# Kernel optimization log

Hardware: AMD Instinct MI355X
Metric: run time of the kernel (lower is better)

The kernel has to match this reference:

```python
import jax, jax.numpy as jnp
import numpy as np
from jax import lax

B, C, H, W = 32, 64, 56, 56
G = 4            # num_heads*2 with num_heads=2
SMK, K = 5, 7
C2 = C // 2
HEAD_DIM = C // G
SCALE = HEAD_DIM ** -0.5


def _bias_idx(k, h, w):
    # static replica of ContMix.generate_idx + apply_rpb index construction
    rpb_size = 2 * k - 1
    idx_h = np.arange(k)
    idx_w = np.arange(k)
    idx_k = (idx_h[:, None] * rpb_size + idx_w).reshape(-1)
    rep_h = np.ones(k, np.int64); rep_h[k // 2] = h - (k - 1)
    rep_w = np.ones(k, np.int64); rep_w[k // 2] = w - (k - 1)
    bias_hw = np.repeat(idx_h, rep_h)[:, None] * rpb_size + np.repeat(idx_w, rep_w)  # (h, w)
    bias_idx = (bias_hw[..., None] + idx_k).reshape(-1, k * k)[::-1]  # torch.flip dim 0
    return jnp.asarray(bias_idx.copy())

IDX1 = _bias_idx(SMK, H, W)
IDX2 = _bias_idx(K, H, W)


def setup_inputs() -> dict:
    key = jax.random.key(0)
    ks = jax.random.split(key, 18)
    r = lambda i, sh: jax.random.normal(ks[i], sh, jnp.float32)
    return dict(
        x=r(0, (B, C, H, W)),
        lepe_w=r(1, (C, 1, K, K)) * 0.1,
        lepe_b=r(2, (C,)) * 0.1,
        lepe_bn_s=1.0 + 0.1 * r(3, (C,)),
        lepe_bn_b=0.1 * r(4, (C,)),
        wq_w=r(5, (C2, C2)) * (C2 ** -0.5),
        wq_bn_s=1.0 + 0.1 * r(6, (C2,)),
        wq_bn_b=0.1 * r(7, (C2,)),
        wk_w=r(8, (C2, C2)) * (C2 ** -0.5),
        wk_bn_s=1.0 + 0.1 * r(9, (C2,)),
        wk_bn_b=0.1 * r(10, (C2,)),
        wp_w=r(11, (SMK * SMK + K * K, 49)) * (49 ** -0.5),
        wp_b=0.1 * r(12, (SMK * SMK + K * K,)),
        rpb1=0.02 * r(13, (G, 2 * SMK - 1, 2 * SMK - 1)),
        rpb2=0.02 * r(14, (G, 2 * K - 1, 2 * K - 1)),
        dy_w=r(15, (C, C)) * (C ** -0.5),
        dy_bn_s=1.0 + 0.1 * r(16, (C,)),
        dy_bn_b=0.1 * r(17, (C,)),
    )


def _per_ch(t):
    return t[None, :, None, None]


def _contmix(x, lepe_w, lepe_b, lepe_bn_s, lepe_bn_b, wq_w, wq_bn_s, wq_bn_b,
             wk_w, wk_bn_s, wk_bn_b, wp_w, wp_b, rpb1, rpb2, dy_w, dy_bn_s, dy_bn_b):
    # lepe: deploy-mode DilatedReparamBlock = depthwise 7x7 conv (+bias), then eval BN
    lepe = lax.conv_general_dilated(x, lepe_w, (1, 1), [(K // 2, K // 2)] * 2,
                                    feature_group_count=C)
    lepe = (lepe + _per_ch(lepe_b)) * _per_ch(lepe_bn_s) + _per_ch(lepe_bn_b)

    q, kf = jnp.split(x, 2, axis=1)                         # (B, C2, H, W) each
    q = jnp.einsum('oi,bihw->bohw', wq_w, q)                # weight_query 1x1 conv
    q = (q * _per_ch(wq_bn_s) + _per_ch(wq_bn_b)) * SCALE
    # weight_key: AdaptiveAvgPool2d(7) -> 1x1 conv -> BN (H,W divisible by 7)
    kp = kf.reshape(B, C2, 7, H // 7, 7, W // 7).mean(axis=(3, 5))
    kp = jnp.einsum('oi,bihw->bohw', wk_w, kp)
    kp = kp * _per_ch(wk_bn_s) + _per_ch(wk_bn_b)

    qg = q.reshape(B, G, C2 // G, H * W)                    # b g c n
    kg = kp.reshape(B, G, C2 // G, 49)                      # b g c l
    w = jnp.einsum('bgcn,bgcl->bgnl', qg, kg)               # (B, G, HW, 49)
    # weight_proj: 1x1 conv over the 49 pooled-context channels
    w = jnp.einsum('ml,bgnl->bgnm', wp_w, w) + wp_b         # (B, G, HW, 74)
    w = w.reshape(B, G, H, W, SMK * SMK + K * K)

    attn1 = w[..., :SMK * SMK]
    attn2 = w[..., SMK * SMK:]
    attn1 = attn1 + rpb1.reshape(G, -1)[:, IDX1].reshape(1, G, H, W, SMK * SMK)
    attn2 = attn2 + rpb2.reshape(G, -1)[:, IDX2].reshape(1, G, H, W, K * K)
    attn1 = jax.nn.softmax(attn1, axis=-1)
    attn2 = jax.nn.softmax(attn2, axis=-1)

    c = C // (2 * G)                                        # value head dim = 8
    v = x.reshape(B, 2, G, c, H, W)                         # 'b (m g c) h w'

    def dyn_mix(attn, val, k):
        # unfold + einsum: content-adaptive depthwise mixing
        p = lax.conv_general_dilated_patches(
            val.reshape(B, G * c, H, W), (k, k), (1, 1), [(k // 2, k // 2)] * 2,
            dimension_numbers=('NCHW', 'OIHW', 'NCHW'))
        p = p.reshape(B, G, c, k * k, H, W)                 # channel-major patch layout
        return jnp.einsum('bgckhw,bghwk->bgchw', p, attn)

    x1 = dyn_mix(attn1, v[:, 0], SMK)
    x2 = dyn_mix(attn2, v[:, 1], K)
    out = jnp.concatenate([x1, x2], axis=1).reshape(B, C, H, W)
    out = jnp.einsum('oi,bihw->bohw', dy_w, out)            # dyconv_proj 1x1 + BN
    out = out * _per_ch(dy_bn_s) + _per_ch(dy_bn_b)
    return out + lepe


def reference(x, lepe_w, lepe_b, lepe_bn_s, lepe_bn_b, wq_w, wq_bn_s, wq_bn_b,
              wk_w, wk_bn_s, wk_bn_b, wp_w, wp_b, rpb1, rpb2, dy_w, dy_bn_s, dy_bn_b):
    return _contmix(x, lepe_w, lepe_b, lepe_bn_s, lepe_bn_b, wq_w, wq_bn_s, wq_bn_b,
                    wk_w, wk_bn_s, wk_bn_b, wp_w, wp_b, rpb1, rpb2, dy_w, dy_bn_s, dy_bn_b)
```

## Files before the change

### kernel.cpp

```cpp
#include <hip/hip_runtime.h>

#define BB 32
#define CC 64
#define HH 56
#define WW 56
#define HW 3136
#define TW 64
#define TR 12

__global__ __launch_bounds__(256) void prep_k(const float* __restrict__ x,
                                              const float* __restrict__ wk,
                                              const float* __restrict__ wks,
                                              const float* __restrict__ wkb,
                                              const float* __restrict__ wp_w,
                                              float* __restrict__ WK) {
    __shared__ float p_s[32 * 49];
    __shared__ float kg_s[8 * 49];
    const int b = blockIdx.x >> 2;
    const int g = blockIdx.x & 3;
    const int tid = threadIdx.x;
    for (int idx = tid; idx < 1568; idx += 256) {
        const int i = idx / 49, l = idx % 49;
        const int py = l / 7, px = l % 7;
        const float4* xp4 = reinterpret_cast<const float4*>(
            x + ((long)(b * CC + 32 + i)) * HW + py * 8 * WW + px * 8);
        float4 sA = make_float4(0.f, 0.f, 0.f, 0.f);
        float4 sB = make_float4(0.f, 0.f, 0.f, 0.f);
        #pragma unroll
        for (int y = 0; y < 8; ++y) {
            const float4 a = xp4[y * 14];
            const float4 c = xp4[y * 14 + 1];
            sA.x += a.x; sA.y += a.y; sA.z += a.z; sA.w += a.w;
            sB.x += c.x; sB.y += c.y; sB.z += c.z; sB.w += c.w;
        }
        p_s[idx] = (sA.x + sA.y + sA.z + sA.w + sB.x + sB.y + sB.z + sB.w) * (1.f / 64.f);
    }
    __syncthreads();
    for (int idx = tid; idx < 392; idx += 256) {
        const int o8 = idx / 49, l = idx % 49;
        const int o = g * 8 + o8;
        float acc = 0.f;
        #pragma unroll
        for (int i = 0; i < 32; ++i) acc = fmaf(wk[o * 32 + i], p_s[i * 49 + l], acc);
        kg_s[idx] = acc * wks[o] + wkb[o];
    }
    __syncthreads();
    for (int idx = tid; idx < 640; idx += 256) {
        const int c = idx / 80, slot = idx % 80;
        float acc = 0.f;
        int m = -1;
        if (slot < 28) { if (slot < 25) m = slot; }
        else           { if (slot < 77) m = 25 + (slot - 28); }
        if (m >= 0) {
            const float* kp = kg_s + c * 49;
            #pragma unroll
            for (int l = 0; l < 49; ++l) acc = fmaf(wp_w[m * 49 + l], kp[l], acc);
        }
        const long base = (long)blockIdx.x * 640;
        if (slot < 28) WK[base + c * 28 + slot] = acc;
        else           WK[base + 224 + c * 52 + (slot - 28)] = acc;
    }
}

__global__ __launch_bounds__(256) void attnmix_k(const float* __restrict__ x,
                                                 const float* __restrict__ WK,
                                                 const float* __restrict__ wq_w,
                                                 const float* __restrict__ wq_s,
                                                 const float* __restrict__ wq_bb,
                                                 const float* __restrict__ wp_b,
                                                 const float* __restrict__ rpb1,
                                                 const float* __restrict__ rpb2,
                                                 const float* __restrict__ lw,
                                                 const float* __restrict__ lb,
                                                 const float* __restrict__ ls,
                                                 const float* __restrict__ lbb,
                                                 float* __restrict__ mix,
                                                 float* __restrict__ out) {
    __shared__ float tile[8 * TR * TW];
    __shared__ float WK1_s[8 * 28];
    __shared__ float WK2_s[8 * 52];
    __shared__ float wqT_s[32 * 8];
    __shared__ float wpb1_s[25];
    __shared__ float wpb2_s[49];
    __shared__ float rpb1_s[81];
    __shared__ float rpb2_s[169];
    __shared__ float wqbn_s[16];
    __shared__ float lw_s[16 * 49];
    __shared__ float lbn_s[48];
    const int tid = threadIdx.x;
    const int bg = blockIdx.y;
    const int g = bg & 3, b = bg >> 2;

    {
        const float* wkp = WK + (long)bg * 640;
        for (int i = tid; i < 224; i += 256) WK1_s[i] = wkp[i];
        for (int i = tid; i < 416; i += 256) WK2_s[i] = wkp[224 + i];
    }
    {
        const int i = tid >> 3, c = tid & 7;
        wqT_s[tid] = wq_w[(g * 8 + c) * 32 + i];
    }
    if (tid < 25) wpb1_s[tid] = wp_b[tid];
    if (tid >= 32 && tid < 81) wpb2_s[tid - 32] = wp_b[25 + tid - 32];
    if (tid < 81) rpb1_s[tid] = rpb1[g * 81 + tid];
    if (tid < 169) rpb2_s[tid] = rpb2[g * 169 + tid];
    if (tid >= 192 && tid < 200) wqbn_s[tid - 192] = wq_s[g * 8 + tid - 192];
    if (tid >= 200 && tid < 208) wqbn_s[8 + tid - 200] = wq_bb[g * 8 + tid - 200];
    for (int i = tid; i < 784; i += 256) {
        const int ch = i / 49, k = i % 49;
        const int c = (ch < 8) ? (g * 8 + ch) : (32 + g * 8 + ch - 8);
        lw_s[i] = lw[c * 49 + k];
    }
    if (tid < 16) {
        const int c = (tid < 8) ? (g * 8 + tid) : (32 + g * 8 + tid - 8);
        lbn_s[tid] = lb[c]; lbn_s[16 + tid] = ls[c]; lbn_s[32 + tid] = lbb[c];
    }

    const int N0 = blockIdx.x << 8;
    const int ph0 = N0 / WW;
    const int r0 = ph0 - 3;

    {
        const float* xc = x + ((long)b * CC + g * 8) * HW;
        #pragma unroll
        for (int ch = 0; ch < 8; ++ch)
            for (int k = tid; k < TR * TW; k += 256) {
                const int row = k >> 6, lxx = k & 63;
                const int gy = r0 + row, gx = lxx - 3;
                float v = 0.f;
                if ((unsigned)gy < HH && (unsigned)gx < WW) v = xc[ch * HW + gy * WW + gx];
                tile[ch * (TR * TW) + k] = v;
            }
    }
    __syncthreads();

    const int n = N0 + tid;
    const bool valid = n < HW;
    const int nc = valid ? n : HW - 1;
    const int ph = nc / WW, pw = nc % WW;
    const int yr = HH - 1 - ph, xr = WW - 1 - pw;
    const int lrow = ph - r0;
    const int tb0 = (lrow - 3) * TW + pw;

    const float* xb = x + (long)b * CC * HW + nc;

    float q8[8];
    #pragma unroll
    for (int c = 0; c < 8; ++c) q8[c] = 0.f;
    for (int i = 0; i < 32; ++i) {
        const float xv = xb[i * HW];
        #pragma unroll
        for (int c = 0; c < 8; ++c) q8[c] = fmaf(wqT_s[i * 8 + c], xv, q8[c]);
    }
    #pragma unroll
    for (int c = 0; c < 8; ++c)
        q8[c] = (q8[c] * wqbn_s[c] + wqbn_s[8 + c]) * 0.25f;

    __builtin_amdgcn_sched_barrier(0);

    {
        float w1[25];
        #pragma unroll
        for (int m = 0; m < 25; ++m) w1[m] = wpb1_s[m];
        #pragma unroll
        for (int c = 0; c < 8; ++c) {
            const float qv = q8[c];
            #pragma unroll
            for (int m = 0; m < 25; ++m) w1[m] = fmaf(qv, WK1_s[c * 28 + m], w1[m]);
        }
        const int rh5 = yr < 2 ? yr : (yr > 53 ? yr - 51 : 2);
        const int rw5 = xr < 2 ? xr : (xr > 53 ? xr - 51 : 2);
        #pragma unroll
        for (int i = 0; i < 5; ++i)
            #pragma unroll
            for (int j = 0; j < 5; ++j)
                w1[i * 5 + j] += rpb1_s[(rh5 + i) * 9 + (rw5 + j)];
        float mx = -1e30f;
        #pragma unroll
        for (int m = 0; m < 25; ++m) mx = fmaxf(mx, w1[m]);
        float sm = 0.f;
        #pragma unroll
        for (int m = 0; m < 25; ++m) { w1[m] = __expf(w1[m] - mx); sm += w1[m]; }
        const float r = 1.f / sm;
        #pragma unroll
        for (int m = 0; m < 25; ++m) w1[m] *= r;

        float* m0 = mix + ((long)b * CC + g * 8) * HW + nc;
        float* o0 = out + ((long)b * CC + g * 8) * HW + nc;
        #pragma unroll
        for (int ch = 0; ch < 8; ++ch) {
            const float* t = tile + ch * (TR * TW) + tb0;
            const float* lwc = lw_s + ch * 49;
            float a = 0.f, la = 0.f;
            #pragma unroll
            for (int i = 0; i < 7; ++i)
                #pragma unroll
                for (int j = 0; j < 7; ++j) {
                    const float v = t[i * TW + j];
                    la = fmaf(lwc[i * 7 + j], v, la);
                    if (i >= 1 && i <= 5 && j >= 1 && j <= 5)
                        a = fmaf(w1[(i - 1) * 5 + (j - 1)], v, a);
                }
            if (valid) {
                m0[ch * HW] = a;
                o0[ch * HW] = (la + lbn_s[ch]) * lbn_s[16 + ch] + lbn_s[32 + ch];
            }
        }
    }

    __syncthreads();
    {
        const float* xc = x + ((long)b * CC + 32 + g * 8) * HW;
        #pragma unroll
        for (int ch = 0; ch < 8; ++ch)
            for (int k = tid; k < TR * TW; k += 256) {
                const int row = k >> 6, lxx = k & 63;
                const int gy = r0 + row, gx = lxx - 3;
                float v = 0.f;
                if ((unsigned)gy < HH && (unsigned)gx < WW) v = xc[ch * HW + gy * WW + gx];
                tile[ch * (TR * TW) + k] = v;
            }
    }
    __syncthreads();

    {
        float w2[49];
        #pragma unroll
        for (int m = 0; m < 49; ++m) w2[m] = wpb2_s[m];
        #pragma unroll
        for (int c = 0; c < 8; ++c) {
            const float qv = q8[c];
            #pragma unroll
            for (int m = 0; m < 49; ++m) w2[m] = fmaf(qv, WK2_s[c * 52 + m], w2[m]);
        }
        const int rh7 = yr < 3 ? yr : (yr > 52 ? yr - 49 : 3);
        const int rw7 = xr < 3 ? xr : (xr > 52 ? xr - 49 : 3);
        #pragma unroll
        for (int i = 0; i < 7; ++i)
            #pragma unroll
            for (int j = 0; j < 7; ++j)
                w2[i * 7 + j] += rpb2_s[(rh7 + i) * 13 + (rw7 + j)];
        float mx = -1e30f;
        #pragma unroll
        for (int m = 0; m < 49; ++m) mx = fmaxf(mx, w2[m]);
        float sm = 0.f;
        #pragma unroll
        for (int m = 0; m < 49; ++m) { w2[m] = __expf(w2[m] - mx); sm += w2[m]; }
        const float r = 1.f / sm;
        #pragma unroll
        for (int m = 0; m < 49; ++m) w2[m] *= r;

        float* m1 = mix + ((long)b * CC + 32 + g * 8) * HW + nc;
        float* o1 = out + ((long)b * CC + 32 + g * 8) * HW + nc;
        #pragma unroll
        for (int ch = 0; ch < 8; ++ch) {
            const float* t = tile + ch * (TR * TW) + tb0;
            const float* lwc = lw_s + (8 + ch) * 49;
            float a = 0.f, la = 0.f;
            #pragma unroll
            for (int i = 0; i < 7; ++i)
                #pragma unroll
                for (int j = 0; j < 7; ++j) {
                    const float v = t[i * TW + j];
                    la = fmaf(lwc[i * 7 + j], v, la);
                    a = fmaf(w2[i * 7 + j], v, a);
                }
            if (valid) {
                m1[ch * HW] = a;
                o1[ch * HW] = (la + lbn_s[8 + ch]) * lbn_s[16 + 8 + ch] + lbn_s[32 + 8 + ch];
            }
        }
    }
}

__global__ __launch_bounds__(256) void final_k(const float* __restrict__ mix,
                                               const float* __restrict__ dy_w,
                                               const float* __restrict__ s,
                                               const float* __restrict__ bb,
                                               float* __restrict__ out) {
    __shared__ float w_s[64 * 64];
    const int tid = threadIdx.x;
    const int b = blockIdx.y;
    for (int i = tid; i < 4096; i += 256) w_s[(i & 63) * 64 + (i >> 6)] = dy_w[i];
    __syncthreads();
    const int oo = (tid >> 5) * 8;
    const int p4 = blockIdx.x * 32 + (tid & 31);
    if (p4 >= 784) return;
    const float* mp = mix + (long)b * CC * HW + p4 * 4;
    float4 acc[8];
    #pragma unroll
    for (int o = 0; o < 8; ++o) acc[o] = make_float4(0.f, 0.f, 0.f, 0.f);
    for (int i = 0; i < 64; ++i) {
        const float4 mv = *reinterpret_cast<const float4*>(mp + (long)i * HW);
        const float* wr = w_s + i * 64 + oo;
        #pragma unroll
        for (int o = 0; o < 8; ++o) {
            const float wv = wr[o];
            acc[o].x = fmaf(wv, mv.x, acc[o].x);
            acc[o].y = fmaf(wv, mv.y, acc[o].y);
            acc[o].z = fmaf(wv, mv.z, acc[o].z);
            acc[o].w = fmaf(wv, mv.w, acc[o].w);
        }
    }
    float* op = out + (long)b * CC * HW + p4 * 4;
    #pragma unroll
    for (int o = 0; o < 8; ++o) {
        const float sc = s[oo + o], bc = bb[oo + o];
        float4* dst = reinterpret_cast<float4*>(op + (long)(oo + o) * HW);
        float4 prev = *dst;
        prev.x = fmaf(acc[o].x, sc, bc) + prev.x;
        prev.y = fmaf(acc[o].y, sc, bc) + prev.y;
        prev.z = fmaf(acc[o].z, sc, bc) + prev.z;
        prev.w = fmaf(acc[o].w, sc, bc) + prev.w;
        *dst = prev;
    }
}

extern "C" void kernel_launch(void* const* d_in, const int* in_sizes, int n_in,
                              void* d_out, int out_size, void* d_ws, size_t ws_size,
                              hipStream_t stream) {
    const float* x       = (const float*)d_in[0];
    const float* lepe_w  = (const float*)d_in[1];
    const float* lepe_b  = (const float*)d_in[2];
    const float* lepe_s  = (const float*)d_in[3];
    const float* lepe_bb = (const float*)d_in[4];
    const float* wq_w    = (const float*)d_in[5];
    const float* wq_s    = (const float*)d_in[6];
    const float* wq_bb   = (const float*)d_in[7];
    const float* wk_w    = (const float*)d_in[8];
    const float* wk_s    = (const float*)d_in[9];
    const float* wk_bb   = (const float*)d_in[10];
    const float* wp_w    = (const float*)d_in[11];
    const float* wp_b    = (const float*)d_in[12];
    const float* rpb1    = (const float*)d_in[13];
    const float* rpb2    = (const float*)d_in[14];
    const float* dy_w    = (const float*)d_in[15];
    const float* dy_s    = (const float*)d_in[16];
    const float* dy_bb   = (const float*)d_in[17];
    float* out = (float*)d_out;

    float* ws     = (float*)d_ws;
    float* WK_ws  = ws;
    float* mix_ws = WK_ws + 128 * 640;

    const int nTiles = (HW + 255) / 256;

    prep_k<<<dim3(BB * 4), 256, 0, stream>>>(x, wk_w, wk_s, wk_bb, wp_w, WK_ws);
    attnmix_k<<<dim3(nTiles, BB * 4), 256, 0, stream>>>(x, WK_ws, wq_w, wq_s, wq_bb,
                                                        wp_b, rpb1, rpb2,
                                                        lepe_w, lepe_b, lepe_s, lepe_bb,
                                                        mix_ws, out);
    final_k<<<dim3(25, BB), 256, 0, stream>>>(mix_ws, dy_w, dy_s, dy_bb, out);
}
```

Baseline: 245.2 us.

## Use channel-interleaved swizzled LDS tile and vectorized weight reads in attnmix

Changes the shared-memory input tile from channel-planar to a pixel-major layout with 8 channels interleaved and XOR-swizzled, so each 7x7 tap loads all 8 channels with two float4 LDS reads. Depthwise and dynamic-mix weights are transposed so they too are read as float4. Projection and bias arrays are padded for float4 loads, and the 1x1 projection kernel batches eight global loads before its FMAs. This aims to cut LDS instruction count and hide global load latency, at the cost of 16 live accumulators per thread and higher register pressure.

Result: slower. 284.9 us (+16.2%).

```diff
diff --git a/kernel.cpp b/kernel.cpp
--- a/kernel.cpp
+++ b/kernel.cpp
@@ -76,63 +76,55 @@
                                                  const float* __restrict__ lbb,
                                                  float* __restrict__ mix,
                                                  float* __restrict__ out) {
-    __shared__ float tile[8 * TR * TW];
-    __shared__ float WK1_s[8 * 28];
-    __shared__ float WK2_s[8 * 52];
-    __shared__ float wqT_s[32 * 8];
-    __shared__ float wpb1_s[25];
-    __shared__ float wpb2_s[49];
+    __shared__ __align__(16) float tile[TR * TW * 8];
+    __shared__ __align__(16) float WK_s[640];
+    __shared__ __align__(16) float wp_s[80];
+    __shared__ __align__(16) float wqT_s[1024];
+    __shared__ __align__(16) float lwT_s[784];
     __shared__ float rpb1_s[81];
     __shared__ float rpb2_s[169];
     __shared__ float wqbn_s[16];
-    __shared__ float lw_s[16 * 49];
     __shared__ float lbn_s[48];
     const int tid = threadIdx.x;
     const int bg = blockIdx.y;
     const int g = bg & 3, b = bg >> 2;
 
     {
-        const float* wkp = WK + (long)bg * 640;
-        for (int i = tid; i < 224; i += 256) WK1_s[i] = wkp[i];
-        for (int i = tid; i < 416; i += 256) WK2_s[i] = wkp[224 + i];
-    }
-    {
         const int i = tid >> 3, c = tid & 7;
         wqT_s[tid] = wq_w[(g * 8 + c) * 32 + i];
-    }
-    if (tid < 25) wpb1_s[tid] = wp_b[tid];
-    if (tid >= 32 && tid < 81) wpb2_s[tid - 32] = wp_b[25 + tid - 32];
+        wqT_s[256 + tid] = 0.f;
+        wqT_s[512 + tid] = 0.f;
+        wqT_s[768 + tid] = 0.f;
+    }
+    {
+        const float* wkp = WK + (long)bg * 640;
+        for (int i = tid; i < 640; i += 256) WK_s[i] = wkp[i];
+    }
+    if (tid < 80) {
+        int m = -1;
+        if (tid < 28) { if (tid < 25) m = tid; }
+        else          { if (tid < 77) m = 25 + (tid - 28); }
+        wp_s[tid] = (m >= 0) ? wp_b[m] : 0.f;
+    }
+    for (int i = tid; i < 784; i += 256) {
+        const int phs = i / 392, rem = i % 392;
+        const int tap = rem >> 3, ch = rem & 7;
+        const int c = (phs ? 32 : 0) + g * 8 + ch;
+        lwT_s[i] = lw[c * 49 + tap];
+    }
     if (tid < 81) rpb1_s[tid] = rpb1[g * 81 + tid];
-    if (tid < 169) rpb2_s[tid] = rpb2[g * 169 + tid];
+    if (tid >= 81 && tid < 250) rpb2_s[tid - 81] = rpb2[g * 169 + (tid - 81)];
     if (tid >= 192 && tid < 200) wqbn_s[tid - 192] = wq_s[g * 8 + tid - 192];
     if (tid >= 200 && tid < 208) wqbn_s[8 + tid - 200] = wq_bb[g * 8 + tid - 200];
-    for (int i = tid; i < 784; i += 256) {
-        const int ch = i / 49, k = i % 49;
-        const int c = (ch < 8) ? (g * 8 + ch) : (32 + g * 8 + ch - 8);
-        lw_s[i] = lw[c * 49 + k];
-    }
-    if (tid < 16) {
-        const int c = (tid < 8) ? (g * 8 + tid) : (32 + g * 8 + tid - 8);
-        lbn_s[tid] = lb[c]; lbn_s[16 + tid] = ls[c]; lbn_s[32 + tid] = lbb[c];
+    if (tid >= 208 && tid < 224) {
+        const int c16 = tid - 208;
+        const int c = (c16 < 8) ? (g * 8 + c16) : (32 + g * 8 + (c16 - 8));
+        lbn_s[c16] = lb[c]; lbn_s[16 + c16] = ls[c]; lbn_s[32 + c16] = lbb[c];
     }
 
     const int N0 = blockIdx.x << 8;
     const int ph0 = N0 / WW;
     const int r0 = ph0 - 3;
-
-    {
-        const float* xc = x + ((long)b * CC + g * 8) * HW;
-        #pragma unroll
-        for (int ch = 0; ch < 8; ++ch)
-            for (int k = tid; k < TR * TW; k += 256) {
-                const int row = k >> 6, lxx = k & 63;
-                const int gy = r0 + row, gx = lxx - 3;
-                float v = 0.f;
-                if ((unsigned)gy < HH && (unsigned)gx < WW) v = xc[ch * HW + gy * WW + gx];
-                tile[ch * (TR * TW) + k] = v;
-            }
-    }
-    __syncthreads();
 
     const int n = N0 + tid;
     const bool valid = n < HW;
@@ -144,29 +136,63 @@
 
     const float* xb = x + (long)b * CC * HW + nc;
 
+    {
+        const float* xc = x + ((long)b * CC + g * 8) * HW;
+        for (int k = tid; k < TR * TW; k += 256) {
+            const int row = k >> 6, col = k & 63;
+            const int gy = r0 + row, gx = col - 3;
+            const bool in = ((unsigned)gy < HH) && ((unsigned)gx < WW);
+            const float* src = xc + gy * WW + gx;
+            float v[8];
+            #pragma unroll
+            for (int ch = 0; ch < 8; ++ch) v[ch] = in ? src[ch * HW] : 0.f;
+            const int e = (k << 3) ^ (k & 12);
+            *reinterpret_cast<float4*>(tile + e)       = make_float4(v[0], v[1], v[2], v[3]);
+            *reinterpret_cast<float4*>(tile + (e ^ 4)) = make_float4(v[4], v[5], v[6], v[7]);
+        }
+    }
+    __syncthreads();
+
     float q8[8];
     #pragma unroll
     for (int c = 0; c < 8; ++c) q8[c] = 0.f;
+    #pragma unroll 8
     for (int i = 0; i < 32; ++i) {
         const float xv = xb[i * HW];
-        #pragma unroll
-        for (int c = 0; c < 8; ++c) q8[c] = fmaf(wqT_s[i * 8 + c], xv, q8[c]);
+        const float4 wA = *reinterpret_cast<const float4*>(wqT_s + i * 8);
+        const float4 wB = *reinterpret_cast<const float4*>(wqT_s + i * 8 + 4);
+        q8[0] = fmaf(wA.x, xv, q8[0]); q8[1] = fmaf(wA.y, xv, q8[1]);
+        q8[2] = fmaf(wA.z, xv, q8[2]); q8[3] = fmaf(wA.w, xv, q8[3]);
+        q8[4] = fmaf(wB.x, xv, q8[4]); q8[5] = fmaf(wB.y, xv, q8[5]);
+        q8[6] = fmaf(wB.z, xv, q8[6]); q8[7] = fmaf(wB.w, xv, q8[7]);
     }
     #pragma unroll
     for (int c = 0; c < 8; ++c)
         q8[c] = (q8[c] * wqbn_s[c] + wqbn_s[8 + c]) * 0.25f;
 
-    __builtin_amdgcn_sched_barrier(0);
-
-    {
-        float w1[25];
-        #pragma unroll
-        for (int m = 0; m < 25; ++m) w1[m] = wpb1_s[m];
+    {
+        float w1[28];
+        {
+            const float4* wp4 = reinterpret_cast<const float4*>(wp_s);
+            #pragma unroll
+            for (int qd = 0; qd < 7; ++qd) {
+                const float4 bv = wp4[qd];
+                w1[qd * 4 + 0] = bv.x; w1[qd * 4 + 1] = bv.y;
+                w1[qd * 4 + 2] = bv.z; w1[qd * 4 + 3] = bv.w;
+            }
+        }
         #pragma unroll
         for (int c = 0; c < 8; ++c) {
             const float qv = q8[c];
-            #pragma unroll
-            for (int m = 0; m < 25; ++m) w1[m] = fmaf(qv, WK1_s[c * 28 + m], w1[m]);
+            const float4* kr = reinterpret_cast<const float4*>(WK_s + c * 28);
+            #pragma unroll
+            for (int qd = 0; qd < 7; ++qd) {
+                const float4 kv = kr[qd];
+                w1[qd * 4 + 0] = fmaf(qv, kv.x, w1[qd * 4 + 0]);
+                w1[qd * 4 + 1] = fmaf(qv, kv.y, w1[qd * 4 + 1]);
+                w1[qd * 4 + 2] = fmaf(qv, kv.z, w1[qd * 4 + 2]);
+                w1[qd * 4 + 3] = fmaf(qv, kv.w, w1[qd * 4 + 3]);
+            }
         }
         const int rh5 = yr < 2 ? yr : (yr > 53 ? yr - 51 : 2);
         const int rw5 = xr < 2 ? xr : (xr > 53 ? xr - 51 : 2);
@@ -185,25 +211,40 @@
         #pragma unroll
         for (int m = 0; m < 25; ++m) w1[m] *= r;
 
-        float* m0 = mix + ((long)b * CC + g * 8) * HW + nc;
-        float* o0 = out + ((long)b * CC + g * 8) * HW + nc;
-        #pragma unroll
-        for (int ch = 0; ch < 8; ++ch) {
-            const float* t = tile + ch * (TR * TW) + tb0;
-            const float* lwc = lw_s + ch * 49;
-            float a = 0.f, la = 0.f;
-            #pragma unroll
-            for (int i = 0; i < 7; ++i)
-                #pragma unroll
-                for (int j = 0; j < 7; ++j) {
-                    const float v = t[i * TW + j];
-                    la = fmaf(lwc[i * 7 + j], v, la);
-                    if (i >= 1 && i <= 5 && j >= 1 && j <= 5)
-                        a = fmaf(w1[(i - 1) * 5 + (j - 1)], v, a);
+        float a[8], la[8];
+        #pragma unroll
+        for (int c = 0; c < 8; ++c) { a[c] = 0.f; la[c] = 0.f; }
+        #pragma unroll
+        for (int i = 0; i < 7; ++i) {
+            const int prow = tb0 + i * TW;
+            #pragma unroll
+            for (int j = 0; j < 7; ++j) {
+                const int p = prow + j;
+                const int e = (p << 3) ^ (p & 12);
+                const float4 v0 = *reinterpret_cast<const float4*>(tile + e);
+                const float4 v1 = *reinterpret_cast<const float4*>(tile + (e ^ 4));
+                const float4 l0 = *reinterpret_cast<const float4*>(lwT_s + (i * 7 + j) * 8);
+                const float4 l1 = *reinterpret_cast<const float4*>(lwT_s + (i * 7 + j) * 8 + 4);
+                la[0] = fmaf(l0.x, v0.x, la[0]); la[1] = fmaf(l0.y, v0.y, la[1]);
+                la[2] = fmaf(l0.z, v0.z, la[2]); la[3] = fmaf(l0.w, v0.w, la[3]);
+                la[4] = fmaf(l1.x, v1.x, la[4]); la[5] = fmaf(l1.y, v1.y, la[5]);
+                la[6] = fmaf(l1.z, v1.z, la[6]); la[7] = fmaf(l1.w, v1.w, la[7]);
+                if (i >= 1 && i <= 5 && j >= 1 && j <= 5) {
+                    const float w = w1[(i - 1) * 5 + (j - 1)];
+                    a[0] = fmaf(w, v0.x, a[0]); a[1] = fmaf(w, v0.y, a[1]);
+                    a[2] = fmaf(w, v0.z, a[2]); a[3] = fmaf(w, v0.w, a[3]);
+                    a[4] = fmaf(w, v1.x, a[4]); a[5] = fmaf(w, v1.y, a[5]);
+                    a[6] = fmaf(w, v1.z, a[6]); a[7] = fmaf(w, v1.w, a[7]);
                 }
-            if (valid) {
-                m0[ch * HW] = a;
-                o0[ch * HW] = (la + lbn_s[ch]) * lbn_s[16 + ch] + lbn_s[32 + ch];
+            }
+        }
+        if (valid) {
+            float* m0 = mix + ((long)b * CC + g * 8) * HW + nc;
+            float* o0 = out + ((long)b * CC + g * 8) * HW + nc;
+            #pragma unroll
+            for (int ch = 0; ch < 8; ++ch) {
+                m0[ch * HW] = a[ch];
+                o0[ch * HW] = (la[ch] + lbn_s[ch]) * lbn_s[16 + ch] + lbn_s[32 + ch];
             }
         }
     }
@@ -211,27 +252,44 @@
     __syncthreads();
     {
         const float* xc = x + ((long)b * CC + 32 + g * 8) * HW;
-        #pragma unroll
-        for (int ch = 0; ch < 8; ++ch)
-            for (int k = tid; k < TR * TW; k += 256) {
-                const int row = k >> 6, lxx = k & 63;
-                const int gy = r0 + row, gx = lxx - 3;
-                float v = 0.f;
-                if ((unsigned)gy < HH && (unsigned)gx < WW) v = xc[ch * HW + gy * WW + gx];
-                tile[ch * (TR * TW) + k] = v;
-            }
-    }
-    __syncthreads();
-
-    {
-        float w2[49];
-        #pragma unroll
-        for (int m = 0; m < 49; ++m) w2[m] = wpb2_s[m];
+        for (int k = tid; k < TR * TW; k += 256) {
+            const int row = k >> 6, col = k & 63;
+            const int gy = r0 + row, gx = col - 3;
+            const bool in = ((unsigned)gy < HH) && ((unsigned)gx < WW);
+            const float* src = xc + gy * WW + gx;
+            float v[8];
+            #pragma unroll
+            for (int ch = 0; ch < 8; ++ch) v[ch] = in ? src[ch * HW] : 0.f;
+            const int e = (k << 3) ^ (k & 12);
+            *reinterpret_cast<float4*>(tile + e)       = make_float4(v[0], v[1], v[2], v[3]);
+            *reinterpret_cast<float4*>(tile + (e ^ 4)) = make_float4(v[4], v[5], v[6], v[7]);
+        }
+    }
+    __syncthreads();
+
+    {
+        float w2[52];
+        {
+            const float4* wp4 = reinterpret_cast<const float4*>(wp_s + 28);
+            #pragma unroll
+            for (int qd = 0; qd < 13; ++qd) {
+                const float4 bv = wp4[qd];
+                w2[qd * 4 + 0] = bv.x; w2[qd * 4 + 1] = bv.y;
+                w2[qd * 4 + 2] = bv.z; w2[qd * 4 + 3] = bv.w;
+            }
+        }
         #pragma unroll
         for (int c = 0; c < 8; ++c) {
             const float qv = q8[c];
-            #pragma unroll
-            for (int m = 0; m < 49; ++m) w2[m] = fmaf(qv, WK2_s[c * 52 + m], w2[m]);
+            const float4* kr = reinterpret_cast<const float4*>(WK_s + 224 + c * 52);
+            #pragma unroll
+            for (int qd = 0; qd < 13; ++qd) {
+                const float4 kv = kr[qd];
+                w2[qd * 4 + 0] = fmaf(qv, kv.x, w2[qd * 4 + 0]);
+                w2[qd * 4 + 1] = fmaf(qv, kv.y, w2[qd * 4 + 1]);
+                w2[qd * 4 + 2] = fmaf(qv, kv.z, w2[qd * 4 + 2]);
+                w2[qd * 4 + 3] = fmaf(qv, kv.w, w2[qd * 4 + 3]);
+            }
         }
         const int rh7 = yr < 3 ? yr : (yr > 52 ? yr - 49 : 3);
         const int rw7 = xr < 3 ? xr : (xr > 52 ? xr - 49 : 3);
@@ -250,24 +308,38 @@
         #pragma unroll
         for (int m = 0; m < 49; ++m) w2[m] *= r;
 
-        float* m1 = mix + ((long)b * CC + 32 + g * 8) * HW + nc;
-        float* o1 = out + ((long)b * CC + 32 + g * 8) * HW + nc;
-        #pragma unroll
-        for (int ch = 0; ch < 8; ++ch) {
-            const float* t = tile + ch * (TR * TW) + tb0;
-            const float* lwc = lw_s + (8 + ch) * 49;
-            float a = 0.f, la = 0.f;
-            #pragma unroll
-            for (int i = 0; i < 7; ++i)
-                #pragma unroll
-                for (int j = 0; j < 7; ++j) {
-                    const float v = t[i * TW + j];
-                    la = fmaf(lwc[i * 7 + j], v, la);
-                    a = fmaf(w2[i * 7 + j], v, a);
-                }
-            if (valid) {
-                m1[ch * HW] = a;
-                o1[ch * HW] = (la + lbn_s[8 + ch]) * lbn_s[16 + 8 + ch] + lbn_s[32 + 8 + ch];
+        float a[8], la[8];
+        #pragma unroll
+        for (int c = 0; c < 8; ++c) { a[c] = 0.f; la[c] = 0.f; }
+        #pragma unroll
+        for (int i = 0; i < 7; ++i) {
+            const int prow = tb0 + i * TW;
+            #pragma unroll
+            for (int j = 0; j < 7; ++j) {
+                const int p = prow + j;
+                const int e = (p << 3) ^ (p & 12);
+                const float4 v0 = *reinterpret_cast<const float4*>(tile + e);
+                const float4 v1 = *reinterpret_cast<const float4*>(tile + (e ^ 4));
+                const float4 l0 = *reinterpret_cast<const float4*>(lwT_s + 392 + (i * 7 + j) * 8);
+                const float4 l1 = *reinterpret_cast<const float4*>(lwT_s + 392 + (i * 7 + j) * 8 + 4);
+                const float w = w2[i * 7 + j];
+                la[0] = fmaf(l0.x, v0.x, la[0]); la[1] = fmaf(l0.y, v0.y, la[1]);
+                la[2] = fmaf(l0.z, v0.z, la[2]); la[3] = fmaf(l0.w, v0.w, la[3]);
+                la[4] = fmaf(l1.x, v1.x, la[4]); la[5] = fmaf(l1.y, v1.y, la[5]);
+                la[6] = fmaf(l1.z, v1.z, la[6]); la[7] = fmaf(l1.w, v1.w, la[7]);
+                a[0] = fmaf(w, v0.x, a[0]); a[1] = fmaf(w, v0.y, a[1]);
+                a[2] = fmaf(w, v0.z, a[2]); a[3] = fmaf(w, v0.w, a[3]);
+                a[4] = fmaf(w, v1.x, a[4]); a[5] = fmaf(w, v1.y, a[5]);
+                a[6] = fmaf(w, v1.z, a[6]); a[7] = fmaf(w, v1.w, a[7]);
+            }
+        }
+        if (valid) {
+            float* m1 = mix + ((long)b * CC + 32 + g * 8) * HW + nc;
+            float* o1 = out + ((long)b * CC + 32 + g * 8) * HW + nc;
+            #pragma unroll
+            for (int ch = 0; ch < 8; ++ch) {
+                m1[ch * HW] = a[ch];
+                o1[ch * HW] = (la[ch] + lbn_s[8 + ch]) * lbn_s[24 + ch] + lbn_s[40 + ch];
             }
         }
     }
@@ -290,16 +362,22 @@
     float4 acc[8];
     #pragma unroll
     for (int o = 0; o < 8; ++o) acc[o] = make_float4(0.f, 0.f, 0.f, 0.f);
-    for (int i = 0; i < 64; ++i) {
-        const float4 mv = *reinterpret_cast<const float4*>(mp + (long)i * HW);
-        const float* wr = w_s + i * 64 + oo;
-        #pragma unroll
-        for (int o = 0; o < 8; ++o) {
-            const float wv = wr[o];
-            acc[o].x = fmaf(wv, mv.x, acc[o].x);
-            acc[o].y = fmaf(wv, mv.y, acc[o].y);
-            acc[o].z = fmaf(wv, mv.z, acc[o].z);
-            acc[o].w = fmaf(wv, mv.w, acc[o].w);
+    for (int ii = 0; ii < 64; ii += 8) {
+        float4 mv[8];
+        #pragma unroll
+        for (int u = 0; u < 8; ++u)
+            mv[u] = *reinterpret_cast<const float4*>(mp + (long)(ii + u) * HW);
+        #pragma unroll
+        for (int u = 0; u < 8; ++u) {
+            const float* wr = w_s + (ii + u) * 64 + oo;
+            #pragma unroll
+            for (int o = 0; o < 8; ++o) {
+                const float wv = wr[o];
+                acc[o].x = fmaf(wv, mv[u].x, acc[o].x);
+                acc[o].y = fmaf(wv, mv[u].y, acc[o].y);
+                acc[o].z = fmaf(wv, mv[u].z, acc[o].z);
+                acc[o].w = fmaf(wv, mv[u].w, acc[o].w);
+            }
         }
     }
     float* op = out + (long)b * CC * HW + p4 * 4;
```

## Split pooling out of prep kernel, halve lepe weight smem, batch mix loads

Applied to the files above, without the earlier changes.

The pooling stage of the prep kernel moves into its own pool_k kernel. Before, each of 128 blocks recomputed the pool for all 32 channels of its batch, repeating the same work 4 times per batch. Now pool_k computes it once per batch, and the new wk_k reads the pooled result from a workspace buffer. In attnmix, the lepe weight shared buffer is halved and reloaded for the second half, which lowers shared memory use. In final_k, eight channel loads are issued before the FMAs to expose memory-level parallelism. The cost is one extra kernel launch and a global round-trip for the pooled data.

Result: no change. 245.4 us (+0.1%).

```diff
diff --git a/kernel.cpp b/kernel.cpp
--- a/kernel.cpp
+++ b/kernel.cpp
@@ -8,33 +8,40 @@
 #define TW 64
 #define TR 12
 
-__global__ __launch_bounds__(256) void prep_k(const float* __restrict__ x,
-                                              const float* __restrict__ wk,
-                                              const float* __restrict__ wks,
-                                              const float* __restrict__ wkb,
-                                              const float* __restrict__ wp_w,
-                                              float* __restrict__ WK) {
+__global__ __launch_bounds__(256) void pool_k(const float* __restrict__ x,
+                                              float* __restrict__ pws) {
+    const int py = blockIdx.x;
+    const int b  = blockIdx.y;
+    const int tid = threadIdx.x;
+    if (tid >= 224) return;
+    const int i = tid / 7, px = tid % 7;
+    const float4* xp4 = reinterpret_cast<const float4*>(
+        x + ((long)(b * CC + 32 + i)) * HW + py * 8 * WW + px * 8);
+    float4 sA = make_float4(0.f, 0.f, 0.f, 0.f);
+    float4 sB = make_float4(0.f, 0.f, 0.f, 0.f);
+    #pragma unroll
+    for (int y = 0; y < 8; ++y) {
+        const float4 a = xp4[y * 14];
+        const float4 c = xp4[y * 14 + 1];
+        sA.x += a.x; sA.y += a.y; sA.z += a.z; sA.w += a.w;
+        sB.x += c.x; sB.y += c.y; sB.z += c.z; sB.w += c.w;
+    }
+    pws[(long)b * 1568 + i * 49 + py * 7 + px] =
+        (sA.x + sA.y + sA.z + sA.w + sB.x + sB.y + sB.z + sB.w) * (1.f / 64.f);
+}
+
+__global__ __launch_bounds__(256) void wk_k(const float* __restrict__ pws,
+                                            const float* __restrict__ wk,
+                                            const float* __restrict__ wks,
+                                            const float* __restrict__ wkb,
+                                            const float* __restrict__ wp_w,
+                                            float* __restrict__ WK) {
     __shared__ float p_s[32 * 49];
     __shared__ float kg_s[8 * 49];
     const int b = blockIdx.x >> 2;
     const int g = blockIdx.x & 3;
     const int tid = threadIdx.x;
-    for (int idx = tid; idx < 1568; idx += 256) {
-        const int i = idx / 49, l = idx % 49;
-        const int py = l / 7, px = l % 7;
-        const float4* xp4 = reinterpret_cast<const float4*>(
-            x + ((long)(b * CC + 32 + i)) * HW + py * 8 * WW + px * 8);
-        float4 sA = make_float4(0.f, 0.f, 0.f, 0.f);
-        float4 sB = make_float4(0.f, 0.f, 0.f, 0.f);
-        #pragma unroll
-        for (int y = 0; y < 8; ++y) {
-            const float4 a = xp4[y * 14];
-            const float4 c = xp4[y * 14 + 1];
-            sA.x += a.x; sA.y += a.y; sA.z += a.z; sA.w += a.w;
-            sB.x += c.x; sB.y += c.y; sB.z += c.z; sB.w += c.w;
-        }
-        p_s[idx] = (sA.x + sA.y + sA.z + sA.w + sB.x + sB.y + sB.z + sB.w) * (1.f / 64.f);
-    }
+    for (int idx = tid; idx < 1568; idx += 256) p_s[idx] = pws[(long)b * 1568 + idx];
     __syncthreads();
     for (int idx = tid; idx < 392; idx += 256) {
         const int o8 = idx / 49, l = idx % 49;
@@ -85,7 +92,7 @@
     __shared__ float rpb1_s[81];
     __shared__ float rpb2_s[169];
     __shared__ float wqbn_s[16];
-    __shared__ float lw_s[16 * 49];
+    __shared__ float lw_s[8 * 49];
     __shared__ float lbn_s[48];
     const int tid = threadIdx.x;
     const int bg = blockIdx.y;
@@ -106,11 +113,7 @@
     if (tid < 169) rpb2_s[tid] = rpb2[g * 169 + tid];
     if (tid >= 192 && tid < 200) wqbn_s[tid - 192] = wq_s[g * 8 + tid - 192];
     if (tid >= 200 && tid < 208) wqbn_s[8 + tid - 200] = wq_bb[g * 8 + tid - 200];
-    for (int i = tid; i < 784; i += 256) {
-        const int ch = i / 49, k = i % 49;
-        const int c = (ch < 8) ? (g * 8 + ch) : (32 + g * 8 + ch - 8);
-        lw_s[i] = lw[c * 49 + k];
-    }
+    for (int i = tid; i < 392; i += 256) lw_s[i] = lw[(g * 8) * 49 + i];
     if (tid < 16) {
         const int c = (tid < 8) ? (g * 8 + tid) : (32 + g * 8 + tid - 8);
         lbn_s[tid] = lb[c]; lbn_s[16 + tid] = ls[c]; lbn_s[32 + tid] = lbb[c];
@@ -220,6 +223,7 @@
                 if ((unsigned)gy < HH && (unsigned)gx < WW) v = xc[ch * HW + gy * WW + gx];
                 tile[ch * (TR * TW) + k] = v;
             }
+        for (int i = tid; i < 392; i += 256) lw_s[i] = lw[(32 + g * 8) * 49 + i];
     }
     __syncthreads();
 
@@ -255,7 +259,7 @@
         #pragma unroll
         for (int ch = 0; ch < 8; ++ch) {
             const float* t = tile + ch * (TR * TW) + tb0;
-            const float* lwc = lw_s + (8 + ch) * 49;
+            const float* lwc = lw_s + ch * 49;
             float a = 0.f, la = 0.f;
             #pragma unroll
             for (int i = 0; i < 7; ++i)
@@ -263,7 +267,7 @@
                 for (int j = 0; j < 7; ++j) {
                     const float v = t[i * TW + j];
                     la = fmaf(lwc[i * 7 + j], v, la);
-                    a = fmaf(w2[i * 7 + j], v, a);
+                    a  = fmaf(w2[i * 7 + j], v, a);
                 }
             if (valid) {
                 m1[ch * HW] = a;
@@ -290,16 +294,22 @@
     float4 acc[8];
     #pragma unroll
     for (int o = 0; o < 8; ++o) acc[o] = make_float4(0.f, 0.f, 0.f, 0.f);
-    for (int i = 0; i < 64; ++i) {
-        const float4 mv = *reinterpret_cast<const float4*>(mp + (long)i * HW);
-        const float* wr = w_s + i * 64 + oo;
-        #pragma unroll
-        for (int o = 0; o < 8; ++o) {
-            const float wv = wr[o];
-            acc[o].x = fmaf(wv, mv.x, acc[o].x);
-            acc[o].y = fmaf(wv, mv.y, acc[o].y);
-            acc[o].z = fmaf(wv, mv.z, acc[o].z);
-            acc[o].w = fmaf(wv, mv.w, acc[o].w);
+    for (int ii = 0; ii < 64; ii += 8) {
+        float4 mv[8];
+        #pragma unroll
+        for (int u = 0; u < 8; ++u)
+            mv[u] = *reinterpret_cast<const float4*>(mp + (long)(ii + u) * HW);
+        #pragma unroll
+        for (int u = 0; u < 8; ++u) {
+            const float* wr = w_s + (ii + u) * 64 + oo;
+            #pragma unroll
+            for (int o = 0; o < 8; ++o) {
+                const float wv = wr[o];
+                acc[o].x = fmaf(wv, mv[u].x, acc[o].x);
+                acc[o].y = fmaf(wv, mv[u].y, acc[o].y);
+                acc[o].z = fmaf(wv, mv[u].z, acc[o].z);
+                acc[o].w = fmaf(wv, mv[u].w, acc[o].w);
+            }
         }
     }
     float* op = out + (long)b * CC * HW + p4 * 4;
@@ -342,10 +352,12 @@
     float* ws     = (float*)d_ws;
     float* WK_ws  = ws;
     float* mix_ws = WK_ws + 128 * 640;
+    float* p_ws   = mix_ws + 32 * 64 * HW;
 
     const int nTiles = (HW + 255) / 256;
 
-    prep_k<<<dim3(BB * 4), 256, 0, stream>>>(x, wk_w, wk_s, wk_bb, wp_w, WK_ws);
+    pool_k<<<dim3(7, BB), 256, 0, stream>>>(x, p_ws);
+    wk_k<<<dim3(BB * 4), 256, 0, stream>>>(p_ws, wk_w, wk_s, wk_bb, wp_w, WK_ws);
     attnmix_k<<<dim3(nTiles, BB * 4), 256, 0, stream>>>(x, WK_ws, wq_w, wq_s, wq_bb,
                                                         wp_b, rpb1, rpb2,
                                                         lepe_w, lepe_b, lepe_s, lepe_bb,
```
